# Optimization experiments

Hardware: AMD Instinct MI355X
Metric: run time of the kernel (lower is better)

## Reference

```python
import jax, jax.numpy as jnp
import numpy as np

EPS_NORM = 1e-12   # F.normalize default eps
ERR = 1e-6         # self.err threshold in DEFORM_func
B, NV = 16384, 129
NE = NV - 1


def _normalize(x, axis=-1):
    n = jnp.linalg.norm(x, axis=axis, keepdims=True)
    return x / jnp.maximum(n, EPS_NORM)


def _compute_kb(edges, restEdgeL):
    """Discrete curvature binormal: kb_i = 2 e_{i-1} x e_i / (l_{i-1} l_i + e_{i-1}.e_i); kb_0 = 0."""
    e_prev, e_next = edges[:, :-1], edges[:, 1:]
    denom = restEdgeL[:, :-1] * restEdgeL[:, 1:] + jnp.sum(e_prev * e_next, axis=-1)
    kb_inner = 2.0 * jnp.cross(e_prev, e_next) / denom[..., None]
    return jnp.concatenate([jnp.zeros_like(kb_inner[:, :1]), kb_inner], axis=1)


def _quat_rotate(w, v, x):
    """Rotate x by unit quaternion (w, v): x + 2w (v x x) + 2 v x (v x x)."""
    t = jnp.cross(v, x)
    return x + 2.0 * (w[..., None] * t + jnp.cross(v, t))


def setup_inputs() -> dict:
    key = jax.random.key(0)
    k1, k2, k3 = jax.random.split(key, 3)
    vertices = jax.random.normal(k1, (B, NV, 3), dtype=jnp.float32)
    init_direct = jax.random.normal(k2, (B, 3), dtype=jnp.float32)
    restEdgeL = jax.random.uniform(k3, (B, NE), dtype=jnp.float32, minval=0.5, maxval=1.5)
    return {"vertices": vertices, "init_direct": init_direct, "restEdgeL": restEdgeL}


def reference(vertices, init_direct, restEdgeL):
    # edges of the rod: [B, NE, 3]
    edges = vertices[:, 1:] - vertices[:, :-1]
    e0 = edges[:, 0]

    # compute_u0: first Bishop frame axis perpendicular to e0
    N0 = jnp.cross(e0, init_direct)
    u0 = _normalize(jnp.cross(N0, e0))                    # [B, 3]
    v0 = _normalize(jnp.cross(e0, u0))                    # [B, 3]

    # discrete curvature binormal + rotation angle (half-angle trig via |kb| = 2 tan(phi/2))
    kb = _compute_kb(edges, restEdgeL)                    # [B, NE, 3]
    mag = jnp.sum(kb * kb, axis=-1)                       # [B, NE]
    cosPhi = jnp.sqrt(4.0 / (4.0 + mag))
    sinPhi = jnp.sqrt(mag / (4.0 + mag))
    axis = sinPhi[..., None] * _normalize(kb)             # quaternion vector part [B, NE, 3]

    # sequential parallel transport of the Bishop frame (edges 1..NE-1)
    def step(carry, inp):
        u_prev, v_prev = carry
        w_i, ax_i, e_i = inp                              # [B], [B,3], [B,3]
        u_rot = _quat_rotate(w_i, ax_i, u_prev)
        v_rot = _normalize(jnp.cross(e_i, u_rot))
        cond = (1.0 - w_i <= ERR)[:, None]                # straight segment -> keep previous frame
        u = jnp.where(cond, u_prev, u_rot)
        v = jnp.where(cond, v_prev, v_rot)
        return (u, v), (u, v)

    xs = (jnp.moveaxis(cosPhi[:, 1:], 1, 0),
          jnp.moveaxis(axis[:, 1:], 1, 0),
          jnp.moveaxis(edges[:, 1:], 1, 0))
    _, (us, vs) = jax.lax.scan(step, (u0, v0), xs)

    b_u = jnp.concatenate([u0[:, None], jnp.moveaxis(us, 0, 1)], axis=1)  # [B, NE, 3]
    b_v = jnp.concatenate([v0[:, None], jnp.moveaxis(vs, 0, 1)], axis=1)  # [B, NE, 3]
    return b_u, b_v, kb
```

## Files before the change

### kernel.cpp

```cpp
#include <hip/hip_runtime.h>

namespace {

constexpr int kB  = 16384;
constexpr int kNV = 129;
constexpr int kNE = 128;
constexpr int kRPB = 4;

struct F3 { float x, y, z; };
struct D3 { double x, y, z; };
struct Q4 { float w, x, y, z; };

__device__ __forceinline__ F3 subf(F3 a, F3 b) { return { a.x-b.x, a.y-b.y, a.z-b.z }; }
__device__ __forceinline__ F3 crossf(F3 a, F3 b) {
    return { a.y*b.z - a.z*b.y,
             a.z*b.x - a.x*b.z,
             a.x*b.y - a.y*b.x };
}
__device__ __forceinline__ float dotf(F3 a, F3 b) { return a.x*b.x + a.y*b.y + a.z*b.z; }
__device__ __forceinline__ F3 nrmf(F3 a) {
    const float s = 1.0f / fmaxf(sqrtf(dotf(a, a)), 1e-12f);
    return { a.x*s, a.y*s, a.z*s };
}
__device__ __forceinline__ Q4 qmul(Q4 a, Q4 b) {
    return { a.w*b.w - a.x*b.x - a.y*b.y - a.z*b.z,
             a.w*b.x + a.x*b.w + a.y*b.z - a.z*b.y,
             a.w*b.y - a.x*b.z + a.y*b.w + a.z*b.x,
             a.w*b.z + a.x*b.y - a.y*b.x + a.z*b.w };
}
__device__ __forceinline__ F3 qrot(Q4 q, F3 x) {
    const F3 v  = { q.x, q.y, q.z };
    const F3 t  = crossf(v, x);
    const F3 t2 = crossf(v, t);
    return { x.x + 2.0f*(q.w*t.x + t2.x),
             x.y + 2.0f*(q.w*t.y + t2.y),
             x.z + 2.0f*(q.w*t.z + t2.z) };
}
__device__ __forceinline__ Q4 shflup_q(Q4 a, int d) {
    Q4 r;
    r.w = __shfl_up(a.w, d, 64);
    r.x = __shfl_up(a.x, d, 64);
    r.y = __shfl_up(a.y, d, 64);
    r.z = __shfl_up(a.z, d, 64);
    return r;
}

__global__ __launch_bounds__(256)
void rod_frames_scan_kernel(const float* __restrict__ verts,
                            const float* __restrict__ dinit,
                            const float* __restrict__ restL,
                            float* __restrict__ out)
{
    const int wave = threadIdx.x >> 6;
    const int lane = threadIdx.x & 63;
    const int b = blockIdx.x * kRPB + wave;

    __shared__ float sv[kRPB][kNV*3 + 1];

    const float* V = verts + (size_t)b * (kNV*3);
    for (int k = lane; k < kNV*3; k += 64) sv[wave][k] = V[k];
    __syncthreads();

    auto ldf = [&](int vi) -> F3 {
        return { sv[wave][vi*3+0], sv[wave][vi*3+1], sv[wave][vi*3+2] };
    };
    auto ldd = [&](int vi) -> D3 {
        return { (double)sv[wave][vi*3+0],
                 (double)sv[wave][vi*3+1],
                 (double)sv[wave][vi*3+2] };
    };

    const int i0 = 2*lane, i1 = 2*lane + 1;

    const D3 dA = ldd(i0);
    const D3 dB = ldd(i0+1);
    const D3 dC = ldd(i0+2);
    const D3 eAd = { dB.x-dA.x, dB.y-dA.y, dB.z-dA.z };
    const D3 eBd = { dC.x-dB.x, dC.y-dB.y, dC.z-dB.z };
    const F3 eAf = { (float)eAd.x, (float)eAd.y, (float)eAd.z };
    const F3 eBf = { (float)eBd.x, (float)eBd.y, (float)eBd.z };

    const F3 dvf = { dinit[b*3+0], dinit[b*3+1], dinit[b*3+2] };
    const F3 p0  = ldf(0);
    const F3 p1  = ldf(1);
    const F3 e0f = subf(p1, p0);
    const F3 u0  = nrmf(crossf(crossf(e0f, dvf), e0f));

    const float2 Lp = *(const float2*)(restL + (size_t)b*kNE + i0);
    const double lA = (double)Lp.x;
    const double lB = (double)Lp.y;
    const double lPd = __shfl_up(lB, 1, 64);

    F3  kb0 = {0.f, 0.f, 0.f};
    Q4  q0  = {1.f, 0.f, 0.f, 0.f};
    bool act0 = (lane == 0);
    if (lane > 0) {
        const D3 dP = ldd(i0-1);
        const D3 ePd = { dA.x-dP.x, dA.y-dP.y, dA.z-dP.z };
        const double denom = lPd*lA + (ePd.x*eAd.x + ePd.y*eAd.y + ePd.z*eAd.z);
        const F3 ePf = { (float)ePd.x, (float)ePd.y, (float)ePd.z };
        const F3 c = crossf(ePf, eAf);
        const float rd = 2.0f / (float)denom;
        kb0 = { c.x*rd, c.y*rd, c.z*rd };
        const float mag = dotf(kb0, kb0);
        const float inv = 1.0f / (4.0f + mag);
        const float w   = sqrtf(4.0f * inv);
        if (1.0f - w > 1e-6f) {
            act0 = true;
            const float sp = sqrtf(mag * inv);
            const float as = sp / fmaxf(sqrtf(mag), 1e-12f);
            q0 = { w, kb0.x*as, kb0.y*as, kb0.z*as };
        }
    }

    F3  kb1;
    Q4  q1  = {1.f, 0.f, 0.f, 0.f};
    bool act1 = false;
    {
        const double denom = lA*lB + (eAd.x*eBd.x + eAd.y*eBd.y + eAd.z*eBd.z);
        const F3 c = crossf(eAf, eBf);
        const float rd = 2.0f / (float)denom;
        kb1 = { c.x*rd, c.y*rd, c.z*rd };
        const float mag = dotf(kb1, kb1);
        const float inv = 1.0f / (4.0f + mag);
        const float w   = sqrtf(4.0f * inv);
        if (1.0f - w > 1e-6f) {
            act1 = true;
            const float sp = sqrtf(mag * inv);
            const float as = sp / fmaxf(sqrtf(mag), 1e-12f);
            q1 = { w, kb1.x*as, kb1.y*as, kb1.z*as };
        }
    }

    Q4 s = qmul(q1, q0);
    #pragma unroll
    for (int d = 1; d < 64; d <<= 1) {
        const Q4 t = shflup_q(s, d);
        if (lane >= d) s = qmul(s, t);
    }
    Q4 ex = shflup_q(s, 1);
    if (lane == 0) ex = {1.f, 0.f, 0.f, 0.f};
    const Q4 Qa = qmul(q0, ex);
    const Q4 Qb = s;

    const int a0 = act0 ? i0 : -1;
    const int a1 = act1 ? i1 : -1;
    const int la = max(a0, a1);
    int m = la;
    #pragma unroll
    for (int d = 1; d < 64; d <<= 1) {
        const int t = __shfl_up(m, d, 64);
        if (lane >= d) m = max(m, t);
    }
    int exm = __shfl_up(m, 1, 64);
    if (lane == 0) exm = -1;
    const int j0 = max(exm, a0);
    const int j1 = max(exm, la);

    const F3 uA = qrot(Qa, u0);
    const F3 uB = qrot(Qb, u0);

    auto edge_at = [&](int j) -> F3 {
        return subf(ldf(j+1), ldf(j));
    };
    const F3 vvA = nrmf(crossf(edge_at(j0), uA));
    const F3 vvB = nrmf(crossf(edge_at(j1), uB));

    float* bu  = out + (size_t)b * (kNE*3);
    float* bv  = bu  + (size_t)kB * (kNE*3);
    float* kbo = bv  + (size_t)kB * (kNE*3);
    const int o = 6*lane;

    *(float2*)(bu  + o    ) = make_float2(uA.x, uA.y);
    *(float2*)(bu  + o + 2) = make_float2(uA.z, uB.x);
    *(float2*)(bu  + o + 4) = make_float2(uB.y, uB.z);

    *(float2*)(bv  + o    ) = make_float2(vvA.x, vvA.y);
    *(float2*)(bv  + o + 2) = make_float2(vvA.z, vvB.x);
    *(float2*)(bv  + o + 4) = make_float2(vvB.y, vvB.z);

    *(float2*)(kbo + o    ) = make_float2(kb0.x, kb0.y);
    *(float2*)(kbo + o + 2) = make_float2(kb0.z, kb1.x);
    *(float2*)(kbo + o + 4) = make_float2(kb1.y, kb1.z);
}

}

extern "C" void kernel_launch(void* const* d_in, const int* in_sizes, int n_in,
                              void* d_out, int out_size, void* d_ws, size_t ws_size,
                              hipStream_t stream)
{
    const float* verts = (const float*)d_in[0];
    const float* dinit = (const float*)d_in[1];
    const float* restL = (const float*)d_in[2];
    float* out = (float*)d_out;

    dim3 grid(kB / kRPB);
    dim3 block(64 * kRPB);
    hipLaunchKernelGGL(rod_frames_scan_kernel, grid, block, 0, stream,
                       verts, dinit, restL, out);
}
```

Measured before the change: 32.46 us.

## Drop LDS staging, load vertices directly, use ballot for last-active-edge search

Replaces the shared-memory staging of vertices and the block-wide barrier with direct per-lane global loads of the four needed vertices. The shfl-based max scan that finds the last active edge is replaced by two ballots plus count-leading-zeros. Edge vectors for lanes that hold a frame from an earlier edge are fetched by cross-lane shuffles, and only when some lane needs them. This removes LDS traffic, the __syncthreads, and several shuffle rounds, at the cost of strided, overlapping global loads that depend on caching.

Result: faster. 29.21 us (-10.0%).

```diff
diff --git a/kernel.cpp b/kernel.cpp
--- a/kernel.cpp
+++ b/kernel.cpp
@@ -8,16 +8,15 @@
 constexpr int kRPB = 4;
 
 struct F3 { float x, y, z; };
-struct D3 { double x, y, z; };
 struct Q4 { float w, x, y, z; };
 
-__device__ __forceinline__ F3 subf(F3 a, F3 b) { return { a.x-b.x, a.y-b.y, a.z-b.z }; }
 __device__ __forceinline__ F3 crossf(F3 a, F3 b) {
     return { a.y*b.z - a.z*b.y,
              a.z*b.x - a.x*b.z,
              a.x*b.y - a.y*b.x };
 }
 __device__ __forceinline__ float dotf(F3 a, F3 b) { return a.x*b.x + a.y*b.y + a.z*b.z; }
+__device__ __forceinline__ F3 subf(F3 a, F3 b) { return { a.x-b.x, a.y-b.y, a.z-b.z }; }
 __device__ __forceinline__ F3 nrmf(F3 a) {
     const float s = 1.0f / fmaxf(sqrtf(dotf(a, a)), 1e-12f);
     return { a.x*s, a.y*s, a.z*s };
@@ -43,6 +42,9 @@
     r.y = __shfl_up(a.y, d, 64);
     r.z = __shfl_up(a.z, d, 64);
     return r;
+}
+__device__ __forceinline__ int hbit(unsigned long long m) {
+    return 63 - __builtin_clzll(m);
 }
 
 __global__ __launch_bounds__(256)
@@ -55,50 +57,45 @@
     const int lane = threadIdx.x & 63;
     const int b = blockIdx.x * kRPB + wave;
 
-    __shared__ float sv[kRPB][kNV*3 + 1];
+    const int i0 = 2*lane, i1 = 2*lane + 1;
 
     const float* V = verts + (size_t)b * (kNV*3);
-    for (int k = lane; k < kNV*3; k += 64) sv[wave][k] = V[k];
-    __syncthreads();
-
-    auto ldf = [&](int vi) -> F3 {
-        return { sv[wave][vi*3+0], sv[wave][vi*3+1], sv[wave][vi*3+2] };
-    };
-    auto ldd = [&](int vi) -> D3 {
-        return { (double)sv[wave][vi*3+0],
-                 (double)sv[wave][vi*3+1],
-                 (double)sv[wave][vi*3+2] };
-    };
-
-    const int i0 = 2*lane, i1 = 2*lane + 1;
-
-    const D3 dA = ldd(i0);
-    const D3 dB = ldd(i0+1);
-    const D3 dC = ldd(i0+2);
-    const D3 eAd = { dB.x-dA.x, dB.y-dA.y, dB.z-dA.z };
-    const D3 eBd = { dC.x-dB.x, dC.y-dB.y, dC.z-dB.z };
-    const F3 eAf = { (float)eAd.x, (float)eAd.y, (float)eAd.z };
-    const F3 eBf = { (float)eBd.x, (float)eBd.y, (float)eBd.z };
-
-    const F3 dvf = { dinit[b*3+0], dinit[b*3+1], dinit[b*3+2] };
-    const F3 p0  = ldf(0);
-    const F3 p1  = ldf(1);
+    const int pidx = (lane > 0 ? i0-1 : 0) * 3;
+    const F3 vP = { V[pidx  ], V[pidx+1], V[pidx+2] };
+    const F3 vA = { V[i0*3  ], V[i0*3+1], V[i0*3+2] };
+    const F3 vB = { V[i0*3+3], V[i0*3+4], V[i0*3+5] };
+    const F3 vC = { V[i0*3+6], V[i0*3+7], V[i0*3+8] };
+
+    const double eAdx = (double)vB.x - (double)vA.x;
+    const double eAdy = (double)vB.y - (double)vA.y;
+    const double eAdz = (double)vB.z - (double)vA.z;
+    const double eBdx = (double)vC.x - (double)vB.x;
+    const double eBdy = (double)vC.y - (double)vB.y;
+    const double eBdz = (double)vC.z - (double)vB.z;
+    const double ePdx = (double)vA.x - (double)vP.x;
+    const double ePdy = (double)vA.y - (double)vP.y;
+    const double ePdz = (double)vA.z - (double)vP.z;
+    const F3 eAf = { (float)eAdx, (float)eAdy, (float)eAdz };
+    const F3 eBf = { (float)eBdx, (float)eBdy, (float)eBdz };
+    const F3 ePf = { (float)ePdx, (float)ePdy, (float)ePdz };
+
+    const int bw = __builtin_amdgcn_readfirstlane(b);
+    const F3 dvf = { dinit[bw*3+0], dinit[bw*3+1], dinit[bw*3+2] };
+    const F3 p0  = { V[0], V[1], V[2] };
+    const F3 p1  = { V[3], V[4], V[5] };
     const F3 e0f = subf(p1, p0);
     const F3 u0  = nrmf(crossf(crossf(e0f, dvf), e0f));
 
-    const float2 Lp = *(const float2*)(restL + (size_t)b*kNE + i0);
-    const double lA = (double)Lp.x;
-    const double lB = (double)Lp.y;
-    const double lPd = __shfl_up(lB, 1, 64);
+    const float* L = restL + (size_t)b * kNE;
+    const double lP = (double)L[lane > 0 ? i0-1 : 0];
+    const double lA = (double)L[i0];
+    const double lB = (double)L[i1];
 
     F3  kb0 = {0.f, 0.f, 0.f};
     Q4  q0  = {1.f, 0.f, 0.f, 0.f};
     bool act0 = (lane == 0);
     if (lane > 0) {
-        const D3 dP = ldd(i0-1);
-        const D3 ePd = { dA.x-dP.x, dA.y-dP.y, dA.z-dP.z };
-        const double denom = lPd*lA + (ePd.x*eAd.x + ePd.y*eAd.y + ePd.z*eAd.z);
-        const F3 ePf = { (float)ePd.x, (float)ePd.y, (float)ePd.z };
+        const double denom = lP*lA + (ePdx*eAdx + ePdy*eAdy + ePdz*eAdz);
         const F3 c = crossf(ePf, eAf);
         const float rd = 2.0f / (float)denom;
         kb0 = { c.x*rd, c.y*rd, c.z*rd };
@@ -117,7 +114,7 @@
     Q4  q1  = {1.f, 0.f, 0.f, 0.f};
     bool act1 = false;
     {
-        const double denom = lA*lB + (eAd.x*eBd.x + eAd.y*eBd.y + eAd.z*eBd.z);
+        const double denom = lA*lB + (eAdx*eBdx + eAdy*eBdy + eAdz*eBdz);
         const F3 c = crossf(eAf, eBf);
         const float rd = 2.0f / (float)denom;
         kb1 = { c.x*rd, c.y*rd, c.z*rd };
@@ -143,28 +140,30 @@
     const Q4 Qa = qmul(q0, ex);
     const Q4 Qb = s;
 
-    const int a0 = act0 ? i0 : -1;
-    const int a1 = act1 ? i1 : -1;
-    const int la = max(a0, a1);
-    int m = la;
-    #pragma unroll
-    for (int d = 1; d < 64; d <<= 1) {
-        const int t = __shfl_up(m, d, 64);
-        if (lane >= d) m = max(m, t);
-    }
-    int exm = __shfl_up(m, 1, 64);
-    if (lane == 0) exm = -1;
-    const int j0 = max(exm, a0);
-    const int j1 = max(exm, la);
+    const unsigned long long mask0 = __ballot(act0);
+    const unsigned long long mask1 = __ballot(act1);
+    const unsigned long long m0a = mask0 & (~0ull >> (63 - lane));
+    const unsigned long long m1a = lane ? (mask1 & (~0ull >> (64 - lane))) : 0ull;
+    const int j0 = max(2*hbit(m0a), m1a ? 2*hbit(m1a)+1 : -1);
+    const unsigned long long m1b = mask1 & (~0ull >> (63 - lane));
+    const int j1 = max(2*hbit(m0a), m1b ? 2*hbit(m1b)+1 : -1);
 
     const F3 uA = qrot(Qa, u0);
     const F3 uB = qrot(Qb, u0);
 
-    auto edge_at = [&](int j) -> F3 {
-        return subf(ldf(j+1), ldf(j));
-    };
-    const F3 vvA = nrmf(crossf(edge_at(j0), uA));
-    const F3 vvB = nrmf(crossf(edge_at(j1), uB));
+    F3 ej0 = eAf, ej1 = eBf;
+    if (__any((j0 != i0) || (j1 != i1))) {
+        const int s0 = j0 >> 1, s1 = j1 >> 1;
+        const F3 a0 = { __shfl(eAf.x, s0, 64), __shfl(eAf.y, s0, 64), __shfl(eAf.z, s0, 64) };
+        const F3 b0 = { __shfl(eBf.x, s0, 64), __shfl(eBf.y, s0, 64), __shfl(eBf.z, s0, 64) };
+        const F3 a1 = { __shfl(eAf.x, s1, 64), __shfl(eAf.y, s1, 64), __shfl(eAf.z, s1, 64) };
+        const F3 b1 = { __shfl(eBf.x, s1, 64), __shfl(eBf.y, s1, 64), __shfl(eBf.z, s1, 64) };
+        ej0 = (j0 & 1) ? b0 : a0;
+        ej1 = (j1 & 1) ? b1 : a1;
+    }
+
+    const F3 vvA = nrmf(crossf(ej0, uA));
+    const F3 vvB = nrmf(crossf(ej1, uB));
 
     float* bu  = out + (size_t)b * (kNE*3);
     float* bv  = bu  + (size_t)kB * (kNE*3);
```
